# Performance work log

Hardware: AMD Instinct MI355X
Metric: run time of the kernel (lower is better)

Reference implementation:

```python
import jax, jax.numpy as jnp
import numpy as np

B, L, H, V = 8, 512, 256, 32000
ALPHA = 0.95  # EMA coefficient from __init__
LN_EPS = 1e-5
NORM_EPS = 1e-12  # F.normalize eps


def setup_inputs() -> dict:
    key = jax.random.key(0)
    ks = jax.random.split(key, 8)
    g = lambda k, shape, scale: (jax.random.normal(k, shape, jnp.float32) * scale)
    return {
        "seq": jax.random.randint(ks[0], (B, L), 0, V),
        "embed": g(ks[1], (V, H), 0.02),
        "W1": g(ks[2], (H, 2 * H), 1.0 / np.sqrt(H)),
        "b1": jnp.zeros((2 * H,), jnp.float32),
        "W2": g(ks[3], (2 * H, H), 1.0 / np.sqrt(2 * H)),
        "b2": jnp.zeros((H,), jnp.float32),
        "gamma": jnp.ones((H,), jnp.float32),
        "beta": jnp.zeros((H,), jnp.float32),
        "Wrp": g(ks[4], (H, H), 1.0 / np.sqrt(H)),
        "brp": jnp.zeros((H,), jnp.float32),
        "Wout": g(ks[5], (H, V), 1.0 / np.sqrt(H)),
        "bout": jnp.zeros((V,), jnp.float32),
    }


def _encoder(seq, embed, W1, b1, W2, b2, gamma, beta):
    h = embed[seq]  # [B, L, H]
    ff = jnp.maximum(h @ W1 + b1, 0.0) @ W2 + b2  # Linear-ReLU-Linear
    x = h + ff
    mu = x.mean(-1, keepdims=True)
    var = ((x - mu) ** 2).mean(-1, keepdims=True)
    return (x - mu) / jnp.sqrt(var + LN_EPS) * gamma + beta  # LayerNorm


def reference(seq, embed, W1, b1, W2, b2, gamma, beta, Wrp, brp, Wout, bout):
    h = _encoder(seq, embed, W1, b1, W2, b2, gamma, beta)  # [B, L, H]
    b, l, hd = h.shape
    keys = jnp.swapaxes(h[:, :-1, :], 0, 1)  # time-major [L-1, B, H]

    def step(M, k):
        kn = k / jnp.maximum(jnp.linalg.norm(k, axis=-1, keepdims=True), NORM_EPS)
        dv = k - jnp.einsum('bij,bj->bi', M, kn)  # delta: v - M k_hat
        M = M + (1.0 - ALPHA) * jnp.einsum('bi,bj->bij', dv, kn)  # rank-1 update
        return M, None

    M0 = jnp.zeros((b, hd, hd), h.dtype)
    M, _ = jax.lax.scan(step, M0, keys)  # sequential delta-rule recurrence
    m = jnp.einsum('bij,bj->bi', M, h[:, -1, :])  # read-out with last token
    return (m @ Wrp + brp) @ Wout + bout  # [B, V]
```

## Files before the change

kernel.cpp:

```cpp
#include <hip/hip_runtime.h>

constexpr int Bz  = 8;
constexpr int Lz  = 512;
constexpr int Hz  = 256;
constexpr int H2z = 512;
constexpr int Vz  = 32000;
constexpr int Mz  = Bz * Lz;
constexpr float CF = 0.05f;
constexpr int NB  = 16;

typedef __attribute__((ext_vector_type(8))) short bfrag8;
typedef __attribute__((ext_vector_type(4))) float f32x4v;
typedef __attribute__((ext_vector_type(4))) short s4v;

static __device__ __forceinline__ short f2bf(float f) {
  unsigned u = __builtin_bit_cast(unsigned, f);
  u += 0x7fffu + ((u >> 16) & 1u);
  return (short)(u >> 16);
}

static __device__ __forceinline__ void wcvt_tile(
    const float* __restrict__ src, short* __restrict__ dst,
    int K, int N, int n0, int k0, int tid)
{
  __shared__ float tile[64][68];
  const int rr = tid >> 4, c4 = (tid & 15) << 2;
#pragma unroll
  for (int q = 0; q < 4; ++q) {
    const int kr = rr + q * 16;
    *(float4*)&tile[kr][c4] = *(const float4*)(src + (long)(k0 + kr) * N + n0 + c4);
  }
  __syncthreads();
#pragma unroll
  for (int q = 0; q < 4; ++q) {
    const int nr = rr + q * 16;
    s4v o = { f2bf(tile[c4 + 0][nr]), f2bf(tile[c4 + 1][nr]),
              f2bf(tile[c4 + 2][nr]), f2bf(tile[c4 + 3][nr]) };
    *(s4v*)(dst + (long)(n0 + nr) * K + k0 + c4) = o;
  }
}

__global__ __launch_bounds__(256) void k_wcvt2(
    const float* __restrict__ W1, const float* __restrict__ W2,
    short* __restrict__ Wt1, short* __restrict__ Wt2)
{
  const int bx = blockIdx.x, tid = threadIdx.x;
  if (bx < 32) {
    wcvt_tile(W1, Wt1, Hz, H2z, (bx & 7) * 64, (bx >> 3) * 64, tid);
  } else {
    const int b2 = bx - 32;
    wcvt_tile(W2, Wt2, H2z, Hz, (b2 & 3) * 64, (b2 >> 2) * 64, tid);
  }
}

__global__ __launch_bounds__(256) void k_mfma1(
    const int* __restrict__ seq, const float* __restrict__ embed,
    const short* __restrict__ Wt1, const float* __restrict__ b1,
    short* __restrict__ y1bf)
{
  __shared__ short As[64][32];
  __shared__ short Bs[64][32];
  const int tid = threadIdx.x;
  const int n0 = blockIdx.x * 64, m0 = blockIdx.y * 64;
  const int w = tid >> 6, l = tid & 63;
  const int srow = tid >> 2, skq = (tid & 3) << 3;
  const long abase = (long)seq[m0 + srow] * Hz;
  const f32x4v zero = {0.f, 0.f, 0.f, 0.f};
  f32x4v acc[4] = {zero, zero, zero, zero};
  for (int kc = 0; kc < Hz; kc += 32) {
    const float4 a0 = *(const float4*)(embed + abase + kc + skq);
    const float4 a1 = *(const float4*)(embed + abase + kc + skq + 4);
    const bfrag8 bvl = *(const bfrag8*)(Wt1 + (long)(n0 + srow) * Hz + kc + skq);
    __syncthreads();
    bfrag8 av = { f2bf(a0.x), f2bf(a0.y), f2bf(a0.z), f2bf(a0.w),
                  f2bf(a1.x), f2bf(a1.y), f2bf(a1.z), f2bf(a1.w) };
    *(bfrag8*)&As[srow][skq] = av;
    *(bfrag8*)&Bs[srow][skq] = bvl;
    __syncthreads();
    const bfrag8 a = *(const bfrag8*)&As[(w << 4) + (l & 15)][(l >> 4) << 3];
#pragma unroll
    for (int nn = 0; nn < 4; ++nn) {
      const bfrag8 bb = *(const bfrag8*)&Bs[(nn << 4) + (l & 15)][(l >> 4) << 3];
      acc[nn] = __builtin_amdgcn_mfma_f32_16x16x32_bf16(a, bb, acc[nn], 0, 0, 0);
    }
  }
  const int col0 = l & 15, quad = l >> 4;
#pragma unroll
  for (int nn = 0; nn < 4; ++nn) {
    const int col = n0 + (nn << 4) + col0;
    const float bias = b1[col];
#pragma unroll
    for (int i = 0; i < 4; ++i) {
      const int row = m0 + (w << 4) + (quad << 2) + i;
      y1bf[(long)row * H2z + col] = f2bf(fmaxf(acc[nn][i] + bias, 0.0f));
    }
  }
}

__global__ __launch_bounds__(256) void k_mfma2ln(
    const int* __restrict__ seq, const float* __restrict__ embed,
    const short* __restrict__ y1bf, const short* __restrict__ Wt2,
    const float* __restrict__ b2, const float* __restrict__ gamma,
    const float* __restrict__ beta, float* __restrict__ h,
    float* __restrict__ hn, short* __restrict__ Knb)
{
  __shared__ short As[64][32];
  __shared__ short Bs[256][32];
  const int tid = threadIdx.x;
  const int m0 = blockIdx.x * 64;
  const int w = tid >> 6, l = tid & 63;
  const int srow = tid >> 2, skq = (tid & 3) << 3;
  const f32x4v zero = {0.f, 0.f, 0.f, 0.f};
  f32x4v acc[16];
#pragma unroll
  for (int nn = 0; nn < 16; ++nn) acc[nn] = zero;

  for (int kc = 0; kc < H2z; kc += 32) {
    const bfrag8 av = *(const bfrag8*)(y1bf + (long)(m0 + srow) * H2z + kc + skq);
    bfrag8 bv[4];
#pragma unroll
    for (int q = 0; q < 4; ++q)
      bv[q] = *(const bfrag8*)(Wt2 + (long)(srow + (q << 6)) * H2z + kc + skq);
    __syncthreads();
    *(bfrag8*)&As[srow][skq] = av;
#pragma unroll
    for (int q = 0; q < 4; ++q)
      *(bfrag8*)&Bs[srow + (q << 6)][skq] = bv[q];
    __syncthreads();
    const bfrag8 a = *(const bfrag8*)&As[(w << 4) + (l & 15)][(l >> 4) << 3];
#pragma unroll
    for (int nn = 0; nn < 16; ++nn) {
      const bfrag8 bb = *(const bfrag8*)&Bs[(nn << 4) + (l & 15)][(l >> 4) << 3];
      acc[nn] = __builtin_amdgcn_mfma_f32_16x16x32_bf16(a, bb, acc[nn], 0, 0, 0);
    }
  }

  const int col0 = l & 15, quad = l >> 4;
  float g_r[16], be_r[16], b2_r[16];
#pragma unroll
  for (int nn = 0; nn < 16; ++nn) {
    const int col = (nn << 4) + col0;
    g_r[nn] = gamma[col];
    be_r[nn] = beta[col];
    b2_r[nn] = b2[col];
  }
#pragma unroll
  for (int i = 0; i < 4; ++i) {
    const int row = m0 + (w << 4) + (quad << 2) + i;
    const long ebase = (long)seq[row] * Hz;
    float v[16];
    float s = 0.0f, ss = 0.0f;
#pragma unroll
    for (int nn = 0; nn < 16; ++nn) {
      const int col = (nn << 4) + col0;
      const float t = acc[nn][i] + b2_r[nn] + embed[ebase + col];
      v[nn] = t; s += t; ss += t * t;
    }
#pragma unroll
    for (int o = 8; o >= 1; o >>= 1) { s += __shfl_xor(s, o); ss += __shfl_xor(ss, o); }
    const float mu   = s * (1.0f / Hz);
    const float var  = ss * (1.0f / Hz) - mu * mu;
    const float rstd = rsqrtf(var + 1e-5f);
    float hs = 0.0f;
#pragma unroll
    for (int nn = 0; nn < 16; ++nn) {
      const float hv = (v[nn] - mu) * rstd * g_r[nn] + be_r[nn];
      v[nn] = hv; hs += hv * hv;
    }
#pragma unroll
    for (int o = 8; o >= 1; o >>= 1) hs += __shfl_xor(hs, o);
    const float inv = 1.0f / fmaxf(sqrtf(hs), 1e-12f);
    float* hrow  = h  + (long)row * Hz;
    float* hnrow = hn + (long)row * Hz;
    const int bb_ = row >> 9, t = row & 511;
#pragma unroll
    for (int nn = 0; nn < 16; ++nn) {
      const int col = (nn << 4) + col0;
      hrow[col] = v[nn];
      hnrow[col] = v[nn] * inv;
    }
    if (t < 511) {
      short* kr = Knb + ((long)bb_ * 512 + (510 - t)) * Hz;
#pragma unroll
      for (int nn = 0; nn < 16; ++nn) kr[(nn << 4) + col0] = f2bf(v[nn] * inv);
    } else {
      short* kr = Knb + ((long)bb_ * 512 + 511) * Hz;
#pragma unroll
      for (int nn = 0; nn < 16; ++nn) kr[(nn << 4) + col0] = 0;
    }
  }
}

__global__ __launch_bounds__(256) void k_gramT(
    const short* __restrict__ Knb, const float* __restrict__ h,
    const float* __restrict__ hn, float* __restrict__ G,
    float* __restrict__ Wsol, float* __restrict__ p)
{
  const int nb = blockIdx.x, mb = blockIdx.y, b = blockIdx.z;
  __shared__ short As[64][32];
  __shared__ short Bs[64][32];
  __shared__ float Gs2[2][32][33];
  __shared__ float qs[Hz];
  if (nb > mb) {
    const int idx = ((nb * (nb - 1)) >> 1) + mb;
    if (idx >= 16) return;
    const int tid = threadIdx.x;
    qs[tid] = h[((long)b * Lz + 511) * Hz + tid];
    __syncthreads();
    const int s = idx * 32 + (tid >> 3);
    const int g = tid & 7;
    float acc = 0.0f;
    if (s <= 510) {
      const float* src = hn + ((long)b * Lz + (510 - s)) * Hz + (g << 5);
#pragma unroll
      for (int q = 0; q < 8; ++q) {
        const float4 vv = *(const float4*)(src + 4 * q);
        const int c = (g << 5) + 4 * q;
        acc += vv.x * qs[c] + vv.y * qs[c + 1] + vv.z * qs[c + 2] + vv.w * qs[c + 3];
      }
    }
#pragma unroll
    for (int o = 4; o >= 1; o >>= 1) acc += __shfl_xor(acc, o);
    if (g == 0) p[(long)b * 512 + s] = acc;
    return;
  }
  const short* Kb = Knb + (long)b * 512 * Hz;
  const int tid = threadIdx.x;
  const int w = tid >> 6, l = tid & 63;
  const int srow = tid >> 2, skq = (tid & 3) << 3;
  const f32x4v zero = {0.f, 0.f, 0.f, 0.f};
  f32x4v acc[4] = {zero, zero, zero, zero};
  for (int kc = 0; kc < Hz; kc += 32) {
    __syncthreads();
    *(bfrag8*)&As[srow][skq] = *(const bfrag8*)(Kb + (long)(mb * 64 + srow) * Hz + kc + skq);
    *(bfrag8*)&Bs[srow][skq] = *(const bfrag8*)(Kb + (long)(nb * 64 + srow) * Hz + kc + skq);
    __syncthreads();
    const bfrag8 a = *(const bfrag8*)&As[(w << 4) + (l & 15)][(l >> 4) << 3];
#pragma unroll
    for (int nn = 0; nn < 4; ++nn) {
      const bfrag8 bb = *(const bfrag8*)&Bs[(nn << 4) + (l & 15)][(l >> 4) << 3];
      acc[nn] = __builtin_amdgcn_mfma_f32_16x16x32_bf16(a, bb, acc[nn], 0, 0, 0);
    }
  }
  const int col0 = l & 15, quad = l >> 4;
  float* Gb = G + (long)b * 512 * 512;
#pragma unroll
  for (int nn = 0; nn < 4; ++nn) {
    const int col = nb * 64 + (nn << 4) + col0;
#pragma unroll
    for (int i = 0; i < 4; ++i) {
      const int row = mb * 64 + (w << 4) + (quad << 2) + i;
      Gb[(long)row * 512 + col] = acc[nn][i];
    }
  }
  if (mb != nb) return;
#pragma unroll
  for (int nn = 0; nn < 4; ++nn) {
    const int lc = (nn << 4) + col0;
#pragma unroll
    for (int i = 0; i < 4; ++i) {
      const int lr = (w << 4) + (quad << 2) + i;
      if ((lr >> 5) == (lc >> 5)) Gs2[lr >> 5][lr & 31][lc & 31] = acc[nn][i];
    }
  }
  __syncthreads();
  if (w < 2 && l < 32) {
    const int c = l;
    float wv[32];
    wv[0] = (c == 0) ? 1.0f : 0.0f;
#pragma unroll
    for (int i = 1; i < 32; ++i) {
      float sum = 0.0f;
#pragma unroll
      for (int j = 0; j < i; ++j) sum = fmaf(Gs2[w][i][j], wv[j], sum);
      wv[i] = ((i == c) ? 1.0f : 0.0f) - CF * sum;
    }
    const int blk = mb * 2 + w;
    float* dst = Wsol + ((long)(b * NB + blk) << 10) + c;
#pragma unroll
    for (int i = 0; i < 32; ++i) dst[i * 32] = wv[i];
  }
}

__global__ __launch_bounds__(256) void k_solve(
    const float* __restrict__ G, const float* __restrict__ p,
    const float* __restrict__ Wsol, float* __restrict__ d_all)
{
  __shared__ float ds[512];
  __shared__ float part[32][9];
  __shared__ float rhs[32];
  const int b = blockIdx.x, tid = threadIdx.x;
  const int i = tid >> 3, g = tid & 7;
  const float* Gb = G + (long)b * 512 * 512;
  const float* pb = p + (long)b * 512;

  for (int blk = 0; blk < NB; ++blk) {
    float acc0 = 0.0f, acc1 = 0.0f;
    const float* grow = Gb + (long)(blk * 32 + i) * 512 + (g << 2);
    int bp = 0;
    for (; bp + 1 < blk; bp += 2) {
      const float4 g0 = *(const float4*)(grow + bp * 32);
      const float4 g1 = *(const float4*)(grow + bp * 32 + 32);
      const int j0 = bp * 32 + (g << 2), j1 = j0 + 32;
      acc0 += g0.x * ds[j0] + g0.y * ds[j0 + 1] + g0.z * ds[j0 + 2] + g0.w * ds[j0 + 3];
      acc1 += g1.x * ds[j1] + g1.y * ds[j1 + 1] + g1.z * ds[j1 + 2] + g1.w * ds[j1 + 3];
    }
    if (bp < blk) {
      const float4 gv = *(const float4*)(grow + bp * 32);
      const int j = bp * 32 + (g << 2);
      acc0 += gv.x * ds[j] + gv.y * ds[j + 1] + gv.z * ds[j + 2] + gv.w * ds[j + 3];
    }
    part[i][g] = acc0 + acc1;
    __syncthreads();
    if (tid < 32) {
      float c = part[tid][0] + part[tid][1] + part[tid][2] + part[tid][3] +
                part[tid][4] + part[tid][5] + part[tid][6] + part[tid][7];
      rhs[tid] = pb[blk * 32 + tid] - CF * c;
    }
    __syncthreads();
    const float* wrow = Wsol + ((long)(b * NB + blk) << 10) + i * 32 + (g << 2);
    const float4 wv = *(const float4*)wrow;
    const int k0 = g << 2;
    part[i][g] = wv.x * rhs[k0] + wv.y * rhs[k0 + 1] +
                 wv.z * rhs[k0 + 2] + wv.w * rhs[k0 + 3];
    __syncthreads();
    if (tid < 32) {
      float dv = part[tid][0] + part[tid][1] + part[tid][2] + part[tid][3] +
                 part[tid][4] + part[tid][5] + part[tid][6] + part[tid][7];
      if (blk == NB - 1 && tid == 31) dv = 0.0f;
      ds[blk * 32 + tid] = dv;
      d_all[(long)b * 512 + blk * 32 + tid] = dv;
    }
    __syncthreads();
  }
}

__global__ __launch_bounds__(256) void k_mrp(
    const float* __restrict__ h, const float* __restrict__ d_all,
    float* __restrict__ part)
{
  __shared__ float acc_s[4][Hz];
  const int c = blockIdx.x, b = blockIdx.y, tid = threadIdx.x;
  const int w = tid >> 6, lane = tid & 63;
  const float* hb = h + (long)b * Lz * Hz;
  const float* db = d_all + ((long)b << 9);
  const int t0 = c * 16;
  const int off = lane << 2;
  float4 acc = {0.f, 0.f, 0.f, 0.f};
#pragma unroll
  for (int q = 0; q < 4; ++q) {
    const int t = t0 + (q << 2) + w;
    if (t < 511) {
      const float dv = db[510 - t];
      const float4 hv = *(const float4*)(hb + (long)t * Hz + off);
      acc.x = fmaf(dv, hv.x, acc.x); acc.y = fmaf(dv, hv.y, acc.y);
      acc.z = fmaf(dv, hv.z, acc.z); acc.w = fmaf(dv, hv.w, acc.w);
    }
  }
  *(float4*)&acc_s[w][off] = acc;
  __syncthreads();
  if (tid < Hz) {
    part[((long)b * 32 + c) * Hz + tid] =
        acc_s[0][tid] + acc_s[1][tid] + acc_s[2][tid] + acc_s[3][tid];
  }
}

__global__ __launch_bounds__(256) void k_mr2(
    const float* __restrict__ part, const float* __restrict__ Wrp,
    const float* __restrict__ brp, float* __restrict__ r)
{
  __shared__ float ms[Hz];
  const int b = blockIdx.x, tid = threadIdx.x;
  float acc = 0.0f;
#pragma unroll
  for (int c = 0; c < 32; ++c) acc += part[((long)b * 32 + c) * Hz + tid];
  ms[tid] = CF * acc;
  __syncthreads();
  float racc = 0.0f;
#pragma unroll 8
  for (int e = 0; e < Hz; ++e)
    racc = fmaf(ms[e], Wrp[(long)e * Hz + tid], racc);
  r[b * Hz + tid] = racc + brp[tid];
}

__global__ __launch_bounds__(256) void k_outproj(
    const float* __restrict__ r, const float* __restrict__ Wout,
    const float* __restrict__ bout, float* __restrict__ out)
{
  __shared__ float rs[8 * Hz];
  __shared__ float part[4][8][64];
  const int tid = threadIdx.x, w = tid >> 6, lane = tid & 63;
  ((float4*)rs)[tid * 2 + 0] = ((const float4*)r)[tid * 2 + 0];
  ((float4*)rs)[tid * 2 + 1] = ((const float4*)r)[tid * 2 + 1];
  __syncthreads();
  const int col = blockIdx.x * 64 + lane;
  float acc[8] = {};
  const int i0 = w << 6;
#pragma unroll 8
  for (int ii = 0; ii < 64; ++ii) {
    const int i = i0 + ii;
    const float wv = Wout[(long)i * Vz + col];
#pragma unroll
    for (int bb = 0; bb < 8; ++bb) acc[bb] = fmaf(rs[bb * Hz + i], wv, acc[bb]);
  }
#pragma unroll
  for (int bb = 0; bb < 8; ++bb) part[w][bb][lane] = acc[bb];
  __syncthreads();
  const float bo = bout[col];
  float s0 = part[0][w][lane] + part[1][w][lane] + part[2][w][lane] + part[3][w][lane];
  out[(long)w * Vz + col] = s0 + bo;
  const int w4 = w + 4;
  float s1 = part[0][w4][lane] + part[1][w4][lane] + part[2][w4][lane] + part[3][w4][lane];
  out[(long)w4 * Vz + col] = s1 + bo;
}

extern "C" void kernel_launch(void* const* d_in, const int* in_sizes, int n_in,
                              void* d_out, int out_size, void* d_ws, size_t ws_size,
                              hipStream_t stream)
{
  const int*   seq   = (const int*)  d_in[0];
  const float* embed = (const float*)d_in[1];
  const float* W1    = (const float*)d_in[2];
  const float* b1    = (const float*)d_in[3];
  const float* W2    = (const float*)d_in[4];
  const float* b2    = (const float*)d_in[5];
  const float* gamma = (const float*)d_in[6];
  const float* beta  = (const float*)d_in[7];
  const float* Wrp   = (const float*)d_in[8];
  const float* brp   = (const float*)d_in[9];
  const float* Wout  = (const float*)d_in[10];
  const float* bout  = (const float*)d_in[11];
  float* out = (float*)d_out;

  char* ws = (char*)d_ws;
  const size_t MB = 1024u * 1024u;
  short* y1bf = (short*)(ws);
  float* Gf   = (float*)(ws);
  float* hb   = (float*)(ws + 8 * MB);
  float* hnb  = (float*)(ws + 12 * MB);
  short* Knb  = (short*)(ws + 16 * MB);
  short* Wt1  = (short*)(ws + 18 * MB);
  short* Wt2  = (short*)(ws + 18 * MB + 256 * 1024);
  float* Wsol = (float*)(ws + 18 * MB + 512 * 1024);
  float* pbuf = (float*)(ws + 19 * MB);
  float* dall = (float*)(ws + 19 * MB + 16 * 1024);
  float* prt  = (float*)(ws + 19 * MB + 32 * 1024);
  float* rb   = (float*)(ws + 19 * MB + 288 * 1024);

  k_wcvt2<<<64, 256, 0, stream>>>(W1, W2, Wt1, Wt2);
  k_mfma1<<<dim3(H2z / 64, Mz / 64), 256, 0, stream>>>(seq, embed, Wt1, b1, y1bf);
  k_mfma2ln<<<Mz / 64, 256, 0, stream>>>(seq, embed, y1bf, Wt2, b2, gamma, beta,
                                         hb, hnb, Knb);
  k_gramT<<<dim3(8, 8, Bz), 256, 0, stream>>>(Knb, hb, hnb, Gf, Wsol, pbuf);
  k_solve<<<Bz, 256, 0, stream>>>(Gf, pbuf, Wsol, dall);
  k_mrp<<<dim3(32, Bz), 256, 0, stream>>>(hb, dall, prt);
  k_mr2<<<Bz, 256, 0, stream>>>(prt, Wrp, brp, rb);
  k_outproj<<<Vz / 64, 256, 0, stream>>>(rb, Wout, bout, out);
}
```

Measured before the change: 204.6 us.

## Shrink FFN2+LN row tile, fuse M readout kernels, tighten solve step

```diff
diff --git a/kernel.cpp b/kernel.cpp
--- a/kernel.cpp
+++ b/kernel.cpp
@@ -104,89 +104,104 @@
     const float* __restrict__ beta, float* __restrict__ h,
     float* __restrict__ hn, short* __restrict__ Knb)
 {
-  __shared__ short As[64][32];
+  __shared__ short As[16][32];
   __shared__ short Bs[256][32];
+  __shared__ float red[4][16][2];
+  __shared__ float red2[4][16];
   const int tid = threadIdx.x;
-  const int m0 = blockIdx.x * 64;
+  const int m0 = blockIdx.x * 16;
   const int w = tid >> 6, l = tid & 63;
   const int srow = tid >> 2, skq = (tid & 3) << 3;
   const f32x4v zero = {0.f, 0.f, 0.f, 0.f};
-  f32x4v acc[16];
-#pragma unroll
-  for (int nn = 0; nn < 16; ++nn) acc[nn] = zero;
+  f32x4v acc[4] = {zero, zero, zero, zero};
 
   for (int kc = 0; kc < H2z; kc += 32) {
-    const bfrag8 av = *(const bfrag8*)(y1bf + (long)(m0 + srow) * H2z + kc + skq);
+    bfrag8 av = {};
+    if (tid < 64)
+      av = *(const bfrag8*)(y1bf + (long)(m0 + (tid >> 2)) * H2z + kc + skq);
     bfrag8 bv[4];
 #pragma unroll
     for (int q = 0; q < 4; ++q)
       bv[q] = *(const bfrag8*)(Wt2 + (long)(srow + (q << 6)) * H2z + kc + skq);
     __syncthreads();
-    *(bfrag8*)&As[srow][skq] = av;
+    if (tid < 64) *(bfrag8*)&As[tid >> 2][skq] = av;
 #pragma unroll
     for (int q = 0; q < 4; ++q)
       *(bfrag8*)&Bs[srow + (q << 6)][skq] = bv[q];
     __syncthreads();
-    const bfrag8 a = *(const bfrag8*)&As[(w << 4) + (l & 15)][(l >> 4) << 3];
-#pragma unroll
-    for (int nn = 0; nn < 16; ++nn) {
-      const bfrag8 bb = *(const bfrag8*)&Bs[(nn << 4) + (l & 15)][(l >> 4) << 3];
+    const bfrag8 a = *(const bfrag8*)&As[l & 15][(l >> 4) << 3];
+#pragma unroll
+    for (int nn = 0; nn < 4; ++nn) {
+      const bfrag8 bb = *(const bfrag8*)&Bs[(w << 6) + (nn << 4) + (l & 15)][(l >> 4) << 3];
       acc[nn] = __builtin_amdgcn_mfma_f32_16x16x32_bf16(a, bb, acc[nn], 0, 0, 0);
     }
   }
 
   const int col0 = l & 15, quad = l >> 4;
-  float g_r[16], be_r[16], b2_r[16];
-#pragma unroll
-  for (int nn = 0; nn < 16; ++nn) {
-    const int col = (nn << 4) + col0;
-    g_r[nn] = gamma[col];
-    be_r[nn] = beta[col];
-    b2_r[nn] = b2[col];
-  }
+  float g_r[4], be_r[4], b2_r[4];
+#pragma unroll
+  for (int nn = 0; nn < 4; ++nn) {
+    const int col = (w << 6) + (nn << 4) + col0;
+    g_r[nn] = gamma[col]; be_r[nn] = beta[col]; b2_r[nn] = b2[col];
+  }
+
+  float v[4][4];
 #pragma unroll
   for (int i = 0; i < 4; ++i) {
-    const int row = m0 + (w << 4) + (quad << 2) + i;
+    const int lr = (quad << 2) + i;
+    const int row = m0 + lr;
     const long ebase = (long)seq[row] * Hz;
-    float v[16];
     float s = 0.0f, ss = 0.0f;
 #pragma unroll
-    for (int nn = 0; nn < 16; ++nn) {
-      const int col = (nn << 4) + col0;
+    for (int nn = 0; nn < 4; ++nn) {
+      const int col = (w << 6) + (nn << 4) + col0;
       const float t = acc[nn][i] + b2_r[nn] + embed[ebase + col];
-      v[nn] = t; s += t; ss += t * t;
+      v[i][nn] = t; s += t; ss += t * t;
     }
 #pragma unroll
     for (int o = 8; o >= 1; o >>= 1) { s += __shfl_xor(s, o); ss += __shfl_xor(ss, o); }
+    if ((l & 15) == 0) { red[w][lr][0] = s; red[w][lr][1] = ss; }
+  }
+  __syncthreads();
+
+#pragma unroll
+  for (int i = 0; i < 4; ++i) {
+    const int lr = (quad << 2) + i;
+    const float s  = red[0][lr][0] + red[1][lr][0] + red[2][lr][0] + red[3][lr][0];
+    const float ss = red[0][lr][1] + red[1][lr][1] + red[2][lr][1] + red[3][lr][1];
     const float mu   = s * (1.0f / Hz);
     const float var  = ss * (1.0f / Hz) - mu * mu;
     const float rstd = rsqrtf(var + 1e-5f);
     float hs = 0.0f;
 #pragma unroll
-    for (int nn = 0; nn < 16; ++nn) {
-      const float hv = (v[nn] - mu) * rstd * g_r[nn] + be_r[nn];
-      v[nn] = hv; hs += hv * hv;
+    for (int nn = 0; nn < 4; ++nn) {
+      const float hv = (v[i][nn] - mu) * rstd * g_r[nn] + be_r[nn];
+      v[i][nn] = hv; hs += hv * hv;
     }
 #pragma unroll
     for (int o = 8; o >= 1; o >>= 1) hs += __shfl_xor(hs, o);
+    if ((l & 15) == 0) red2[w][lr] = hs;
+  }
+  __syncthreads();
+
+#pragma unroll
+  for (int i = 0; i < 4; ++i) {
+    const int lr = (quad << 2) + i;
+    const float hs = red2[0][lr] + red2[1][lr] + red2[2][lr] + red2[3][lr];
     const float inv = 1.0f / fmaxf(sqrtf(hs), 1e-12f);
+    const int row = m0 + lr;
     float* hrow  = h  + (long)row * Hz;
     float* hnrow = hn + (long)row * Hz;
     const int bb_ = row >> 9, t = row & 511;
-#pragma unroll
-    for (int nn = 0; nn < 16; ++nn) {
-      const int col = (nn << 4) + col0;
-      hrow[col] = v[nn];
-      hnrow[col] = v[nn] * inv;
-    }
-    if (t < 511) {
-      short* kr = Knb + ((long)bb_ * 512 + (510 - t)) * Hz;
-#pragma unroll
-      for (int nn = 0; nn < 16; ++nn) kr[(nn << 4) + col0] = f2bf(v[nn] * inv);
-    } else {
-      short* kr = Knb + ((long)bb_ * 512 + 511) * Hz;
-#pragma unroll
-      for (int nn = 0; nn < 16; ++nn) kr[(nn << 4) + col0] = 0;
+    short* kr = Knb + ((long)bb_ * 512 + (t < 511 ? 510 - t : 511)) * Hz;
+#pragma unroll
+    for (int nn = 0; nn < 4; ++nn) {
+      const int col = (w << 6) + (nn << 4) + col0;
+      const float hv = v[i][nn];
+      const float nv = hv * inv;
+      hrow[col]  = hv;
+      hnrow[col] = nv;
+      kr[col] = (t < 511) ? f2bf(nv) : (short)0;
     }
   }
 }
@@ -313,20 +328,16 @@
     part[i][g] = acc0 + acc1;
     __syncthreads();
     if (tid < 32) {
-      float c = part[tid][0] + part[tid][1] + part[tid][2] + part[tid][3] +
-                part[tid][4] + part[tid][5] + part[tid][6] + part[tid][7];
+      const float c = part[tid][0] + part[tid][1] + part[tid][2] + part[tid][3] +
+                      part[tid][4] + part[tid][5] + part[tid][6] + part[tid][7];
       rhs[tid] = pb[blk * 32 + tid] - CF * c;
-    }
-    __syncthreads();
-    const float* wrow = Wsol + ((long)(b * NB + blk) << 10) + i * 32 + (g << 2);
-    const float4 wv = *(const float4*)wrow;
-    const int k0 = g << 2;
-    part[i][g] = wv.x * rhs[k0] + wv.y * rhs[k0 + 1] +
-                 wv.z * rhs[k0 + 2] + wv.w * rhs[k0 + 3];
-    __syncthreads();
-    if (tid < 32) {
-      float dv = part[tid][0] + part[tid][1] + part[tid][2] + part[tid][3] +
-                 part[tid][4] + part[tid][5] + part[tid][6] + part[tid][7];
+      const float* wrow = Wsol + ((long)(b * NB + blk) << 10) + tid * 32;
+      float dv = 0.0f;
+#pragma unroll
+      for (int k = 0; k < 32; k += 4) {
+        const float4 wv = *(const float4*)(wrow + k);
+        dv += wv.x * rhs[k] + wv.y * rhs[k + 1] + wv.z * rhs[k + 2] + wv.w * rhs[k + 3];
+      }
       if (blk == NB - 1 && tid == 31) dv = 0.0f;
       ds[blk * 32 + tid] = dv;
       d_all[(long)b * 512 + blk * 32 + tid] = dv;
@@ -335,46 +346,28 @@
   }
 }
 
-__global__ __launch_bounds__(256) void k_mrp(
+__global__ __launch_bounds__(256) void k_mrp2(
     const float* __restrict__ h, const float* __restrict__ d_all,
-    float* __restrict__ part)
+    const float* __restrict__ Wrp, const float* __restrict__ brp,
+    float* __restrict__ r)
 {
   __shared__ float acc_s[4][Hz];
-  const int c = blockIdx.x, b = blockIdx.y, tid = threadIdx.x;
+  __shared__ float ms[Hz];
+  const int b = blockIdx.x, tid = threadIdx.x;
   const int w = tid >> 6, lane = tid & 63;
   const float* hb = h + (long)b * Lz * Hz;
   const float* db = d_all + ((long)b << 9);
-  const int t0 = c * 16;
   const int off = lane << 2;
   float4 acc = {0.f, 0.f, 0.f, 0.f};
-#pragma unroll
-  for (int q = 0; q < 4; ++q) {
-    const int t = t0 + (q << 2) + w;
-    if (t < 511) {
-      const float dv = db[510 - t];
-      const float4 hv = *(const float4*)(hb + (long)t * Hz + off);
-      acc.x = fmaf(dv, hv.x, acc.x); acc.y = fmaf(dv, hv.y, acc.y);
-      acc.z = fmaf(dv, hv.z, acc.z); acc.w = fmaf(dv, hv.w, acc.w);
-    }
+  for (int t = w; t < 511; t += 4) {
+    const float dv = db[510 - t];
+    const float4 hv = *(const float4*)(hb + (long)t * Hz + off);
+    acc.x = fmaf(dv, hv.x, acc.x); acc.y = fmaf(dv, hv.y, acc.y);
+    acc.z = fmaf(dv, hv.z, acc.z); acc.w = fmaf(dv, hv.w, acc.w);
   }
   *(float4*)&acc_s[w][off] = acc;
   __syncthreads();
-  if (tid < Hz) {
-    part[((long)b * 32 + c) * Hz + tid] =
-        acc_s[0][tid] + acc_s[1][tid] + acc_s[2][tid] + acc_s[3][tid];
-  }
-}
-
-__global__ __launch_bounds__(256) void k_mr2(
-    const float* __restrict__ part, const float* __restrict__ Wrp,
-    const float* __restrict__ brp, float* __restrict__ r)
-{
-  __shared__ float ms[Hz];
-  const int b = blockIdx.x, tid = threadIdx.x;
-  float acc = 0.0f;
-#pragma unroll
-  for (int c = 0; c < 32; ++c) acc += part[((long)b * 32 + c) * Hz + tid];
-  ms[tid] = CF * acc;
+  ms[tid] = CF * (acc_s[0][tid] + acc_s[1][tid] + acc_s[2][tid] + acc_s[3][tid]);
   __syncthreads();
   float racc = 0.0f;
 #pragma unroll 8
@@ -444,16 +437,14 @@
   float* Wsol = (float*)(ws + 18 * MB + 512 * 1024);
   float* pbuf = (float*)(ws + 19 * MB);
   float* dall = (float*)(ws + 19 * MB + 16 * 1024);
-  float* prt  = (float*)(ws + 19 * MB + 32 * 1024);
-  float* rb   = (float*)(ws + 19 * MB + 288 * 1024);
+  float* rb   = (float*)(ws + 19 * MB + 32 * 1024);
 
   k_wcvt2<<<64, 256, 0, stream>>>(W1, W2, Wt1, Wt2);
   k_mfma1<<<dim3(H2z / 64, Mz / 64), 256, 0, stream>>>(seq, embed, Wt1, b1, y1bf);
-  k_mfma2ln<<<Mz / 64, 256, 0, stream>>>(seq, embed, y1bf, Wt2, b2, gamma, beta,
+  k_mfma2ln<<<Mz / 16, 256, 0, stream>>>(seq, embed, y1bf, Wt2, b2, gamma, beta,
                                          hb, hnb, Knb);
   k_gramT<<<dim3(8, 8, Bz), 256, 0, stream>>>(Knb, hb, hnb, Gf, Wsol, pbuf);
   k_solve<<<Bz, 256, 0, stream>>>(Gf, pbuf, Wsol, dall);
-  k_mrp<<<dim3(32, Bz), 256, 0, stream>>>(hb, dall, prt);
-  k_mr2<<<Bz, 256, 0, stream>>>(prt, Wrp, brp, rb);
+  k_mrp2<<<Bz, 256, 0, stream>>>(hb, dall, Wrp, brp, rb);
   k_outproj<<<Vz / 64, 256, 0, stream>>>(rb, Wout, bout, out);
 }
```

Result: slower. 225.4 us (+10.1%).
